# Kernel tuning notes

Measured on AMD Instinct MI355X. Metric: run time of the kernel, lower is better.

## Reference

```python
import jax, jax.numpy as jnp
import numpy as np

EPS = 1e-6  # T5LayerNorm epsilon


def setup_inputs() -> dict:
    key = jax.random.key(0)
    k0, k1, k2, k3 = jax.random.split(key, 4)
    B, S, D, F, E = 4, 2048, 768, 3072, 8
    hidden_states = jax.random.normal(k0, (B, S, D), jnp.float32)
    router_w = jax.random.normal(k1, (E, D), jnp.float32) * 0.02
    ln_w = jnp.ones((E, D), jnp.float32)
    wi = jax.random.normal(k2, (E, F, D), jnp.float32) * 0.02
    wo = jax.random.normal(k3, (E, D, F), jnp.float32) * 0.02
    return {"hidden_states": hidden_states, "router_w": router_w, "ln_w": ln_w,
            "wi": wi, "wo": wo, "top_k": 2}


def reference(hidden_states, router_w, ln_w, wi, wo, top_k):
    B, S, D = hidden_states.shape
    E = router_w.shape[0]
    x = hidden_states.reshape(-1, D)                      # [T, D] tokens
    router_logits = x @ router_w.T                        # [T, E]
    probs = jax.nn.softmax(router_logits, axis=-1)
    rw, sel = jax.lax.top_k(probs, top_k)                 # [T, K]
    rw = rw / jnp.sum(rw, axis=-1, keepdims=True)         # renormalize top-k weights

    # T5LayerNorm is RMS-norm (no mean subtraction); shared input x, per-expert scale.
    var = jnp.mean(x * x, axis=-1, keepdims=True)         # [T, 1]
    x_norm = x * jax.lax.rsqrt(var + EPS)                 # [T, D]

    out = jnp.zeros_like(x)
    for e in range(E):  # fixed small loop over experts (structurally distinct params)
        # combine weight for expert e: zero for tokens that did not select it
        w_e = jnp.sum(jnp.where(sel == e, rw, 0.0), axis=-1)   # [T]
        h = x_norm * ln_w[e]                                   # [T, D]
        ff = jax.nn.relu(h @ wi[e].T) @ wo[e].T                # [T, D]
        # T5LayerFF returns x + FFN(LN(x)); routing weight scales the whole output
        out = out + w_e[:, None] * (x + ff)
    layer_output = out.reshape(B, S, D)
    return layer_output, router_logits
```

## Files before the change

### kernel.cpp

```cpp
#include <hip/hip_runtime.h>
#include <hip/hip_bf16.h>
#include <math.h>

typedef short short8 __attribute__((ext_vector_type(8)));
typedef float f32x16 __attribute__((ext_vector_type(16)));

constexpr int D = 768;
constexpr int E = 8;
constexpr int F = 3072;
constexpr int T = 8192;
constexpr float EPS = 1e-6f;

static __device__ inline unsigned short f2bf(float f) {
    __hip_bfloat16 h = __float2bfloat16(f);
    return *reinterpret_cast<unsigned short*>(&h);
}

static __device__ inline f32x16 mfma_bf16(short8 a, short8 b, f32x16 c) {
    return __builtin_amdgcn_mfma_f32_32x32x16_bf16(a, b, c, 0, 0, 0);
}

#define GLL16(g, s) __builtin_amdgcn_global_load_lds( \
    (const __attribute__((address_space(1))) unsigned int*)(g), \
    (__attribute__((address_space(3))) unsigned int*)(s), 16, 0, 0)

__global__ __launch_bounds__(256)
void prep_kernel(const float* __restrict__ wi, const float* __restrict__ wo,
                 const float* __restrict__ lnw,
                 unsigned short* __restrict__ wip, unsigned short* __restrict__ wop,
                 const float* __restrict__ x, const float* __restrict__ rw,
                 float* __restrict__ logits, unsigned short* __restrict__ xn,
                 float* __restrict__ out, int* __restrict__ sel,
                 float2* __restrict__ w01)
{
    if (blockIdx.x < 36864) {
        const unsigned NWI = (unsigned)E * F * D;
        unsigned i4 = (blockIdx.x * 256u + threadIdx.x) * 4u;
        if (i4 < NWI) {
            float4 v = *(const float4*)(wi + i4);
            unsigned e = i4 / (unsigned)(F * D);
            unsigned d = i4 % (unsigned)D;
            float4 l = *(const float4*)(lnw + e * D + d);
            ushort4 o = { f2bf(v.x * l.x), f2bf(v.y * l.y), f2bf(v.z * l.z), f2bf(v.w * l.w) };
            *(ushort4*)(wip + i4) = o;
        } else {
            unsigned j = i4 - NWI;
            float4 v = *(const float4*)(wo + j);
            ushort4 o = { f2bf(v.x), f2bf(v.y), f2bf(v.z), f2bf(v.w) };
            *(ushort4*)(wop + j) = o;
        }
        return;
    }

    const int lane = threadIdx.x & 63;
    const int wid  = threadIdx.x >> 6;
    const int t = (blockIdx.x - 36864) * 4 + wid;
    if (t >= T) return;

    const float* xr = x + (size_t)t * D;
    float xv[12];
    float acc[8];
#pragma unroll
    for (int e = 0; e < 8; ++e) acc[e] = 0.f;
    float ssq = 0.f;
#pragma unroll
    for (int i = 0; i < 12; ++i) {
        const int k = lane + 64 * i;
        const float v = xr[k];
        xv[i] = v;
        ssq += v * v;
#pragma unroll
        for (int e = 0; e < 8; ++e) acc[e] += v * rw[e * D + k];
    }
#pragma unroll
    for (int off = 32; off; off >>= 1) {
        ssq += __shfl_xor(ssq, off);
#pragma unroll
        for (int e = 0; e < 8; ++e) acc[e] += __shfl_xor(acc[e], off);
    }

    int e0 = 0; float m0 = acc[0];
#pragma unroll
    for (int e = 1; e < 8; ++e) if (acc[e] > m0) { m0 = acc[e]; e0 = e; }
    int e1 = -1; float m1 = -3.4e38f;
#pragma unroll
    for (int e = 0; e < 8; ++e) if (e != e0 && acc[e] > m1) { m1 = acc[e]; e1 = e; }

    const float r  = expf(m1 - m0);
    const float w0 = 1.f / (1.f + r);
    const float w1 = r * w0;
    const float wsum = w0 + w1;
    const float rs = rsqrtf(ssq * (1.f / (float)D) + EPS);

    if (lane == 0) {
#pragma unroll
        for (int e = 0; e < 8; ++e) logits[t * 8 + e] = acc[e];
        sel[t] = e0 | (e1 << 4);
        w01[t] = make_float2(w0, w1);
    }

#pragma unroll
    for (int i = 0; i < 12; ++i) {
        const int k = lane + 64 * i;
        xn[(size_t)t * D + k] = f2bf(xv[i] * rs);
        out[(size_t)t * D + k] = wsum * xv[i];
    }
}

__global__ __launch_bounds__(256)
void lists_kernel(const int* __restrict__ sel, const float2* __restrict__ w01,
                  int* __restrict__ offs,
                  int* __restrict__ lists, float* __restrict__ wlist)
{
    const int e = blockIdx.x;
    const int tid = threadIdx.x;
    const int lane = tid & 63;
    const int wv = tid >> 6;

    __shared__ int sc[4][8];
    __shared__ int wtot[4];

    int c[8];
#pragma unroll
    for (int i = 0; i < 8; ++i) c[i] = 0;
    for (int t = tid; t < T; t += 256) {
        const int s = sel[t];
        const int a = s & 15, b = (s >> 4) & 15;
#pragma unroll
        for (int i = 0; i < 8; ++i) c[i] += (a == i) + (b == i);
    }
#pragma unroll
    for (int off = 32; off; off >>= 1)
#pragma unroll
        for (int i = 0; i < 8; ++i) c[i] += __shfl_xor(c[i], off);
    if (lane == 0)
#pragma unroll
        for (int i = 0; i < 8; ++i) sc[wv][i] = c[i];
    __syncthreads();

    int cnt8[8];
#pragma unroll
    for (int i = 0; i < 8; ++i) cnt8[i] = sc[0][i] + sc[1][i] + sc[2][i] + sc[3][i];
    int base = 0;
#pragma unroll
    for (int i = 0; i < 8; ++i) if (i < e) base += cnt8[i];

    if (e == 0 && tid == 0) {
        int a = 0;
#pragma unroll
        for (int i = 0; i < 8; ++i) { offs[i] = a; a += cnt8[i]; }
        offs[8] = a;
    }

    int cnt = 0;
    for (int c0 = 0; c0 < T; c0 += 256) {
        const int t = c0 + tid;
        const int s = sel[t];
        const bool m1 = ((s >> 4) & 15) == e;
        const bool m = ((s & 15) == e) || m1;
        const unsigned long long b = __ballot(m);
        const int pre = __popcll(b & ((1ULL << lane) - 1ULL));
        if (lane == 0) wtot[wv] = __popcll(b);
        __syncthreads();
        int wbase = 0;
#pragma unroll
        for (int i = 0; i < 4; ++i) if (i < wv) wbase += wtot[i];
        if (m) {
            const int pos = base + cnt + wbase + pre;
            lists[pos] = (t << 1) | (m1 ? 1 : 0);
            const float2 w = w01[t];
            wlist[pos] = m1 ? w.y : w.x;
        }
        cnt += wtot[0] + wtot[1] + wtot[2] + wtot[3];
        __syncthreads();
    }
}


__global__ __launch_bounds__(256)
void gemm1_kernel(const unsigned short* __restrict__ xn,
                  const unsigned short* __restrict__ wip,
                  const int* __restrict__ offs,
                  const int* __restrict__ lists,
                  unsigned short* __restrict__ H)
{
    __shared__ unsigned short sA[128 * 64];
    __shared__ unsigned short sB[128 * 64];
    __shared__ int s_tok[128];

    const int bid = blockIdx.x;
    const int e  = bid & 7;
    const int q  = bid >> 3;
    const int mt = q / 24;
    const int nt = q % 24;
    const int offe = offs[e];
    const int cnt = offs[e + 1] - offe;
    const int base = mt * 128;
    if (base >= cnt) return;

    const int tid = threadIdx.x;
    const int w = tid >> 6, l = tid & 63;
    const int lo = l & 31, hi = l >> 5;
    const int wr = w >> 1, wc = w & 1;

    if (tid < 128) {
        const int idx = base + tid;
        s_tok[tid] = (idx < cnt) ? (lists[offe + idx] >> 1) : 0;
    }
    __syncthreads();

    const int r = (w * 4 + 0) * 8 + (l >> 3);
    const int chS = ((l & 7) ^ ((l >> 3) & 7)) * 8;
    const unsigned short* aSrc[4];
    const unsigned short* bSrc[4];
#pragma unroll
    for (int j = 0; j < 4; ++j) {
        const int rj = r + j * 8;
        aSrc[j] = xn + (size_t)s_tok[rj] * D + chS;
        bSrc[j] = wip + ((size_t)e * F + nt * 128 + rj) * D + chS;
    }
    char* sAc = (char*)sA;
    char* sBc = (char*)sB;

    f32x16 acc00, acc01, acc10, acc11;
#pragma unroll
    for (int qq = 0; qq < 16; ++qq) { acc00[qq] = 0.f; acc01[qq] = 0.f; acc10[qq] = 0.f; acc11[qq] = 0.f; }

    const int rx = (lo & 7) << 4;
    const int arow0 = (wr * 64 + lo) * 128;
    const int arow1 = arow0 + 32 * 128;
    const int brow0 = (wc * 64 + lo) * 128;
    const int brow1 = brow0 + 32 * 128;

    for (int kt = 0; kt < 12; ++kt) {
        const int k0 = kt * 64;
#pragma unroll
        for (int j = 0; j < 4; ++j) {
            GLL16(aSrc[j] + k0, sAc + (w * 4 + j) * 1024);
            GLL16(bSrc[j] + k0, sBc + (w * 4 + j) * 1024);
        }
        __syncthreads();
#pragma unroll
        for (int ks = 0; ks < 4; ++ks) {
            const int coff = (hi * 16 + ks * 32) ^ rx;
            short8 a0 = *(const short8*)(sAc + arow0 + coff);
            short8 a1 = *(const short8*)(sAc + arow1 + coff);
            short8 b0 = *(const short8*)(sBc + brow0 + coff);
            short8 b1 = *(const short8*)(sBc + brow1 + coff);
            acc00 = mfma_bf16(a0, b0, acc00);
            acc01 = mfma_bf16(a0, b1, acc01);
            acc10 = mfma_bf16(a1, b0, acc10);
            acc11 = mfma_bf16(a1, b1, acc11);
        }
        __syncthreads();
    }

    const int cbase = nt * 128 + wc * 64 + lo;
#pragma unroll
    for (int rr = 0; rr < 16; ++rr) {
        const int crow = (rr & 3) + 8 * (rr >> 2) + 4 * hi;
        int lrow = wr * 64 + crow;
        if (base + lrow < cnt) {
            unsigned short* hp = H + (size_t)(offe + base + lrow) * F + cbase;
            hp[0]  = f2bf(fmaxf(acc00[rr], 0.f));
            hp[32] = f2bf(fmaxf(acc01[rr], 0.f));
        }
        lrow += 32;
        if (base + lrow < cnt) {
            unsigned short* hp = H + (size_t)(offe + base + lrow) * F + cbase;
            hp[0]  = f2bf(fmaxf(acc10[rr], 0.f));
            hp[32] = f2bf(fmaxf(acc11[rr], 0.f));
        }
    }
}

__global__ __launch_bounds__(256)
void gemm2_kernel(const unsigned short* __restrict__ H,
                  const unsigned short* __restrict__ wop,
                  const int* __restrict__ offs,
                  const int* __restrict__ lists, const float* __restrict__ wlist,
                  float* __restrict__ out)
{
    __shared__ unsigned short sA[128 * 64];
    __shared__ unsigned short sB[128 * 64];
    __shared__ int   s_tok[128];
    __shared__ float s_wgt[128];

    const int bid = blockIdx.x;
    const int e  = bid & 7;
    const int q  = bid >> 3;
    const int kh = q / 384;
    const int rm = q % 384;
    const int mt = rm / 6;
    const int nt = rm % 6;
    const int offe = offs[e];
    const int cnt = offs[e + 1] - offe;
    const int base = mt * 128;
    if (base >= cnt) return;

    const int tid = threadIdx.x;
    const int w = tid >> 6, l = tid & 63;
    const int lo = l & 31, hi = l >> 5;
    const int wr = w >> 1, wc = w & 1;

    if (tid < 128) {
        const int idx = base + tid;
        const bool v = idx < cnt;
        s_tok[tid] = v ? lists[offe + idx] : 0;
        s_wgt[tid] = v ? wlist[offe + idx] : 0.f;
    }
    __syncthreads();

    const int r = (w * 4 + 0) * 8 + (l >> 3);
    const int chS = ((l & 7) ^ ((l >> 3) & 7)) * 8;
    const unsigned short* aSrc[4];
    const unsigned short* bSrc[4];
#pragma unroll
    for (int j = 0; j < 4; ++j) {
        const int rj = r + j * 8;
        aSrc[j] = H + (size_t)(offe + base + rj) * F + kh * 1536 + chS;
        bSrc[j] = wop + ((size_t)e * D + nt * 128 + rj) * F + kh * 1536 + chS;
    }
    char* sAc = (char*)sA;
    char* sBc = (char*)sB;

    f32x16 acc00, acc01, acc10, acc11;
#pragma unroll
    for (int qq = 0; qq < 16; ++qq) { acc00[qq] = 0.f; acc01[qq] = 0.f; acc10[qq] = 0.f; acc11[qq] = 0.f; }

    const int rx = (lo & 7) << 4;
    const int arow0 = (wr * 64 + lo) * 128;
    const int arow1 = arow0 + 32 * 128;
    const int brow0 = (wc * 64 + lo) * 128;
    const int brow1 = brow0 + 32 * 128;

    for (int kt = 0; kt < 24; ++kt) {
        const int k0 = kt * 64;
#pragma unroll
        for (int j = 0; j < 4; ++j) {
            GLL16(aSrc[j] + k0, sAc + (w * 4 + j) * 1024);
            GLL16(bSrc[j] + k0, sBc + (w * 4 + j) * 1024);
        }
        __syncthreads();
#pragma unroll
        for (int ks = 0; ks < 4; ++ks) {
            const int coff = (hi * 16 + ks * 32) ^ rx;
            short8 a0 = *(const short8*)(sAc + arow0 + coff);
            short8 a1 = *(const short8*)(sAc + arow1 + coff);
            short8 b0 = *(const short8*)(sBc + brow0 + coff);
            short8 b1 = *(const short8*)(sBc + brow1 + coff);
            acc00 = mfma_bf16(a0, b0, acc00);
            acc01 = mfma_bf16(a0, b1, acc01);
            acc10 = mfma_bf16(a1, b0, acc10);
            acc11 = mfma_bf16(a1, b1, acc11);
        }
        __syncthreads();
    }

    const int cbase = nt * 128 + wc * 64 + lo;
#pragma unroll
    for (int rr = 0; rr < 16; ++rr) {
        const int crow = (rr & 3) + 8 * (rr >> 2) + 4 * hi;
#pragma unroll
        for (int mh = 0; mh < 2; ++mh) {
            const int lrow = wr * 64 + crow + mh * 32;
            if (base + lrow < cnt) {
                const int tk = s_tok[lrow] >> 1;
                const float wgt = s_wgt[lrow];
                float* dst = out + (size_t)tk * D + cbase;
                atomicAdd(dst,      wgt * (mh ? acc10[rr] : acc00[rr]));
                atomicAdd(dst + 32, wgt * (mh ? acc11[rr] : acc01[rr]));
            }
        }
    }
}

extern "C" void kernel_launch(void* const* d_in, const int* in_sizes, int n_in,
                              void* d_out, int out_size, void* d_ws, size_t ws_size,
                              hipStream_t stream) {
    const float* x   = (const float*)d_in[0];
    const float* rw  = (const float*)d_in[1];
    const float* lnw = (const float*)d_in[2];
    const float* wi  = (const float*)d_in[3];
    const float* wo  = (const float*)d_in[4];

    float* out    = (float*)d_out;
    float* logits = (float*)d_out + (size_t)T * D;

    char* ws = (char*)d_ws;
    unsigned short* xn     = (unsigned short*)(ws);
    unsigned short* wip    = (unsigned short*)(ws + 12582912);
    unsigned short* wop    = (unsigned short*)(ws + 50331648);
    unsigned short* H      = (unsigned short*)(ws + 88080384);
    int*            offs   = (int*)(ws + 190316544);
    int*            sel    = (int*)(ws + 190316672);
    float2*         w01    = (float2*)(ws + 190349440);
    int*            lists  = (int*)(ws + 190414976);
    float*          wlist  = (float*)(ws + 190480512);

    prep_kernel<<<36864 + T / 4, 256, 0, stream>>>(wi, wo, lnw, wip, wop,
                                                   x, rw, logits, xn, out,
                                                   sel, w01);

    lists_kernel<<<E, 256, 0, stream>>>(sel, w01, offs, lists, wlist);

    gemm1_kernel<<<64 * 24 * 8, 256, 0, stream>>>(xn, wip, offs, lists, H);
    gemm2_kernel<<<2 * 64 * 6 * 8, 256, 0, stream>>>(H, wop, offs, lists,
                                                     wlist, out);
}
```

Baseline: 336.6 us.

## Replace split-K atomic accumulation in down-projection with per-slot buffer and combine kernel

The second GEMM no longer splits K into two halves. Instead of accumulating with float atomics into the output, it writes each token-slot's weighted FFN result to a dedicated buffer indexed by top-k slot. A new combine kernel then adds both slot buffers into the output, which already holds the residual term. This removes atomic traffic and contention, but halves the number of GEMM2 blocks, doubles each block's K loop, and adds an extra elementwise pass over about 50 MB. The new buffer reuses workspace that held the normalized activations and the packed up-projection weights, which are dead by this point.

```diff
diff --git a/kernel.cpp b/kernel.cpp
--- a/kernel.cpp
+++ b/kernel.cpp
@@ -279,7 +279,7 @@
                   const unsigned short* __restrict__ wop,
                   const int* __restrict__ offs,
                   const int* __restrict__ lists, const float* __restrict__ wlist,
-                  float* __restrict__ out)
+                  float* __restrict__ ffout)
 {
     __shared__ unsigned short sA[128 * 64];
     __shared__ unsigned short sB[128 * 64];
@@ -289,10 +289,8 @@
     const int bid = blockIdx.x;
     const int e  = bid & 7;
     const int q  = bid >> 3;
-    const int kh = q / 384;
-    const int rm = q % 384;
-    const int mt = rm / 6;
-    const int nt = rm % 6;
+    const int mt = q / 6;
+    const int nt = q % 6;
     const int offe = offs[e];
     const int cnt = offs[e + 1] - offe;
     const int base = mt * 128;
@@ -318,8 +316,8 @@
 #pragma unroll
     for (int j = 0; j < 4; ++j) {
         const int rj = r + j * 8;
-        aSrc[j] = H + (size_t)(offe + base + rj) * F + kh * 1536 + chS;
-        bSrc[j] = wop + ((size_t)e * D + nt * 128 + rj) * F + kh * 1536 + chS;
+        aSrc[j] = H + (size_t)(offe + base + rj) * F + chS;
+        bSrc[j] = wop + ((size_t)e * D + nt * 128 + rj) * F + chS;
     }
     char* sAc = (char*)sA;
     char* sBc = (char*)sB;
@@ -334,7 +332,7 @@
     const int brow0 = (wc * 64 + lo) * 128;
     const int brow1 = brow0 + 32 * 128;
 
-    for (int kt = 0; kt < 24; ++kt) {
+    for (int kt = 0; kt < 48; ++kt) {
         const int k0 = kt * 64;
 #pragma unroll
         for (int j = 0; j < 4; ++j) {
@@ -365,14 +363,26 @@
         for (int mh = 0; mh < 2; ++mh) {
             const int lrow = wr * 64 + crow + mh * 32;
             if (base + lrow < cnt) {
-                const int tk = s_tok[lrow] >> 1;
+                const int pk = s_tok[lrow];
                 const float wgt = s_wgt[lrow];
-                float* dst = out + (size_t)tk * D + cbase;
-                atomicAdd(dst,      wgt * (mh ? acc10[rr] : acc00[rr]));
-                atomicAdd(dst + 32, wgt * (mh ? acc11[rr] : acc01[rr]));
+                float* dst = ffout + ((size_t)(pk & 1) * T + (pk >> 1)) * D + cbase;
+                dst[0]  = wgt * (mh ? acc10[rr] : acc00[rr]);
+                dst[32] = wgt * (mh ? acc11[rr] : acc01[rr]);
             }
         }
     }
+}
+
+__global__ __launch_bounds__(256)
+void combine_kernel(const float* __restrict__ ffout, float* __restrict__ out)
+{
+    const long long i4 = ((long long)blockIdx.x * 256 + threadIdx.x) * 4;
+    float4 o  = *(const float4*)(out + i4);
+    float4 f0 = *(const float4*)(ffout + i4);
+    float4 f1 = *(const float4*)(ffout + (long long)T * D + i4);
+    o.x += f0.x + f1.x; o.y += f0.y + f1.y;
+    o.z += f0.z + f1.z; o.w += f0.w + f1.w;
+    *(float4*)(out + i4) = o;
 }
 
 extern "C" void kernel_launch(void* const* d_in, const int* in_sizes, int n_in,
@@ -390,6 +400,7 @@
     char* ws = (char*)d_ws;
     unsigned short* xn     = (unsigned short*)(ws);
     unsigned short* wip    = (unsigned short*)(ws + 12582912);
+    float*          ffout  = (float*)(ws);
     unsigned short* wop    = (unsigned short*)(ws + 50331648);
     unsigned short* H      = (unsigned short*)(ws + 88080384);
     int*            offs   = (int*)(ws + 190316544);
@@ -405,6 +416,7 @@
     lists_kernel<<<E, 256, 0, stream>>>(sel, w01, offs, lists, wlist);
 
     gemm1_kernel<<<64 * 24 * 8, 256, 0, stream>>>(xn, wip, offs, lists, H);
-    gemm2_kernel<<<2 * 64 * 6 * 8, 256, 0, stream>>>(H, wop, offs, lists,
-                                                     wlist, out);
-}
+    gemm2_kernel<<<64 * 6 * 8, 256, 0, stream>>>(H, wop, offs, lists,
+                                                 wlist, ffout);
+    combine_kernel<<<T * D / 4 / 256, 256, 0, stream>>>(ffout, out);
+}
```

Result: faster. 327.2 us (-2.8%).

## Replace gemm2 atomic scatter with per-slot partial buffers and combine pass

Applied to the files above, without the earlier changes.

gemm2 now writes each weighted expert output with plain stores into slot-indexed buffers, one per top-k slot and per K-half, instead of using float atomicAdd into the output. A new combine kernel sums these partial buffers into out. If the workspace is too small, the K split is dropped and each block runs the full K loop. This removes atomic contention and read-modify-write traffic. In exchange it adds large temporary buffers, an extra pass over memory, and possibly less parallelism when the split is off.

```diff
diff --git a/kernel.cpp b/kernel.cpp
--- a/kernel.cpp
+++ b/kernel.cpp
@@ -279,7 +279,8 @@
                   const unsigned short* __restrict__ wop,
                   const int* __restrict__ offs,
                   const int* __restrict__ lists, const float* __restrict__ wlist,
-                  float* __restrict__ out)
+                  float* __restrict__ ffout0, float* __restrict__ ffout1,
+                  int kts)
 {
     __shared__ unsigned short sA[128 * 64];
     __shared__ unsigned short sB[128 * 64];
@@ -311,6 +312,7 @@
     }
     __syncthreads();
 
+    const int kof = kh * kts * 64;
     const int r = (w * 4 + 0) * 8 + (l >> 3);
     const int chS = ((l & 7) ^ ((l >> 3) & 7)) * 8;
     const unsigned short* aSrc[4];
@@ -318,8 +320,8 @@
 #pragma unroll
     for (int j = 0; j < 4; ++j) {
         const int rj = r + j * 8;
-        aSrc[j] = H + (size_t)(offe + base + rj) * F + kh * 1536 + chS;
-        bSrc[j] = wop + ((size_t)e * D + nt * 128 + rj) * F + kh * 1536 + chS;
+        aSrc[j] = H + (size_t)(offe + base + rj) * F + kof + chS;
+        bSrc[j] = wop + ((size_t)e * D + nt * 128 + rj) * F + kof + chS;
     }
     char* sAc = (char*)sA;
     char* sBc = (char*)sB;
@@ -334,7 +336,7 @@
     const int brow0 = (wc * 64 + lo) * 128;
     const int brow1 = brow0 + 32 * 128;
 
-    for (int kt = 0; kt < 24; ++kt) {
+    for (int kt = 0; kt < kts; ++kt) {
         const int k0 = kt * 64;
 #pragma unroll
         for (int j = 0; j < 4; ++j) {
@@ -357,6 +359,7 @@
         __syncthreads();
     }
 
+    float* fbase = kh ? ffout1 : ffout0;
     const int cbase = nt * 128 + wc * 64 + lo;
 #pragma unroll
     for (int rr = 0; rr < 16; ++rr) {
@@ -365,14 +368,33 @@
         for (int mh = 0; mh < 2; ++mh) {
             const int lrow = wr * 64 + crow + mh * 32;
             if (base + lrow < cnt) {
-                const int tk = s_tok[lrow] >> 1;
+                const int pk = s_tok[lrow];
                 const float wgt = s_wgt[lrow];
-                float* dst = out + (size_t)tk * D + cbase;
-                atomicAdd(dst,      wgt * (mh ? acc10[rr] : acc00[rr]));
-                atomicAdd(dst + 32, wgt * (mh ? acc11[rr] : acc01[rr]));
+                float* dst = fbase + ((size_t)(pk & 1) * T + (pk >> 1)) * D + cbase;
+                dst[0]  = wgt * (mh ? acc10[rr] : acc00[rr]);
+                dst[32] = wgt * (mh ? acc11[rr] : acc01[rr]);
             }
         }
     }
+}
+
+__global__ __launch_bounds__(256)
+void combine_kernel(const float* __restrict__ f0, const float* __restrict__ f1,
+                    int nkh, float* __restrict__ out)
+{
+    const long long i4 = ((long long)blockIdx.x * 256 + threadIdx.x) * 4;
+    float4 o  = *(const float4*)(out + i4);
+    float4 a0 = *(const float4*)(f0 + i4);
+    float4 a1 = *(const float4*)(f0 + (long long)T * D + i4);
+    o.x += a0.x + a1.x; o.y += a0.y + a1.y;
+    o.z += a0.z + a1.z; o.w += a0.w + a1.w;
+    if (nkh == 2) {
+        float4 b0 = *(const float4*)(f1 + i4);
+        float4 b1 = *(const float4*)(f1 + (long long)T * D + i4);
+        o.x += b0.x + b1.x; o.y += b0.y + b1.y;
+        o.z += b0.z + b1.z; o.w += b0.w + b1.w;
+    }
+    *(float4*)(out + i4) = o;
 }
 
 extern "C" void kernel_launch(void* const* d_in, const int* in_sizes, int n_in,
@@ -390,6 +412,7 @@
     char* ws = (char*)d_ws;
     unsigned short* xn     = (unsigned short*)(ws);
     unsigned short* wip    = (unsigned short*)(ws + 12582912);
+    float*          ffout0 = (float*)(ws);
     unsigned short* wop    = (unsigned short*)(ws + 50331648);
     unsigned short* H      = (unsigned short*)(ws + 88080384);
     int*            offs   = (int*)(ws + 190316544);
@@ -397,6 +420,11 @@
     float2*         w01    = (float2*)(ws + 190349440);
     int*            lists  = (int*)(ws + 190414976);
     float*          wlist  = (float*)(ws + 190480512);
+    float*          ffout1 = (float*)(ws + 190578688);
+
+    const bool big2 = ws_size >= 240910336ULL;
+    const int nkh = big2 ? 2 : 1;
+    const int kts = 48 / nkh;
 
     prep_kernel<<<36864 + T / 4, 256, 0, stream>>>(wi, wo, lnw, wip, wop,
                                                    x, rw, logits, xn, out,
@@ -405,6 +433,11 @@
     lists_kernel<<<E, 256, 0, stream>>>(sel, w01, offs, lists, wlist);
 
     gemm1_kernel<<<64 * 24 * 8, 256, 0, stream>>>(xn, wip, offs, lists, H);
-    gemm2_kernel<<<2 * 64 * 6 * 8, 256, 0, stream>>>(H, wop, offs, lists,
-                                                     wlist, out);
-}
+    gemm2_kernel<<<nkh * 64 * 6 * 8, 256, 0, stream>>>(H, wop, offs, lists,
+                                                       wlist, ffout0,
+                                                       big2 ? ffout1 : ffout0,
+                                                       kts);
+    combine_kernel<<<T * D / 4 / 256, 256, 0, stream>>>(ffout0,
+                                                        big2 ? ffout1 : ffout0,
+                                                        nkh, out);
+}
```

After: 333.4 us. About the same (-1.0%).
